# Kernel tuning notes

Measured on AMD Instinct MI355X. Metric: run time of the kernel, lower is better.

## Reference

```python
import jax, jax.numpy as jnp
import numpy as np

N_NODES = 100000
N_EDGES = 1600000
F_IN = 128
HIDDEN = 64
OUT = 1
NUM_GRAPHS = 128


def gcn_conv(x, src, dst, W, b, n_nodes):
    """PyG GCNConv: h = x @ W; add self-loops; symmetric deg normalization;
    scatter-add aggregation; + bias."""
    h = x @ W  # [N, H]
    ones = jnp.ones(src.shape[0], dtype=h.dtype)
    # degree on target nodes, +1 for the self-loop
    deg = jax.ops.segment_sum(ones, dst, num_segments=n_nodes) + 1.0  # [N]
    dinv = jax.lax.rsqrt(deg)  # deg^-0.5
    norm = dinv[src] * dinv[dst]  # [E]
    msg = h[src] * norm[:, None]  # gather + normalize, [E, H]
    agg = jax.ops.segment_sum(msg, dst, num_segments=n_nodes)  # scatter-add
    # self-loop contribution: norm_ii = deg_i^-1
    agg = agg + h * (1.0 / deg)[:, None]
    return agg + b


def setup_inputs() -> dict:
    key = jax.random.key(0)
    ks = jax.random.split(key, 8)
    x = jax.random.normal(ks[0], (N_NODES, F_IN), dtype=jnp.float32)
    edge_index = jax.random.randint(ks[1], (2, N_EDGES), 0, N_NODES, dtype=jnp.int64)
    batch = jnp.sort(jax.random.randint(ks[2], (N_NODES,), 0, NUM_GRAPHS, dtype=jnp.int64))
    s1 = 1.0 / np.sqrt(F_IN)
    s2 = 1.0 / np.sqrt(HIDDEN)
    W1 = jax.random.uniform(ks[3], (F_IN, HIDDEN), jnp.float32, -s1, s1)
    b1 = jnp.zeros((HIDDEN,), jnp.float32)
    W2 = jax.random.uniform(ks[4], (HIDDEN, HIDDEN), jnp.float32, -s2, s2)
    b2 = jnp.zeros((HIDDEN,), jnp.float32)
    W_out = jax.random.uniform(ks[5], (HIDDEN, OUT), jnp.float32, -s2, s2)
    b_out = jnp.zeros((OUT,), jnp.float32)
    return {"x": x, "edge_index": edge_index, "batch": batch,
            "W1": W1, "b1": b1, "W2": W2, "b2": b2,
            "W_out": W_out, "b_out": b_out}


def reference(x, edge_index, batch, W1, b1, W2, b2, W_out, b_out):
    n_nodes = x.shape[0]
    src, dst = edge_index[0], edge_index[1]
    h = jax.nn.relu(gcn_conv(x, src, dst, W1, b1, n_nodes))
    h = jax.nn.relu(gcn_conv(h, src, dst, W2, b2, n_nodes))
    # global mean pool over graphs
    sums = jax.ops.segment_sum(h, batch, num_segments=NUM_GRAPHS)  # [G, H]
    counts = jax.ops.segment_sum(jnp.ones(n_nodes, h.dtype), batch, num_segments=NUM_GRAPHS)
    pooled = sums / jnp.maximum(counts, 1.0)[:, None]
    return pooled @ W_out + b_out  # [G, 1]
```

## Files before the change

### kernel.cpp

```cpp
#include <hip/hip_runtime.h>
#include <hip/hip_fp16.h>

#define N_NODES 100000
#define N_EDGES 1600000
#define F_IN 128
#define HID 64
#define NG 128

#define GEMB 1563
#define DEGB 6250
#define CNTB 391
#define NB   391

#define FMA_ROW(acc, xv) \
    acc.x = fmaf(xv.x, w0.x, acc.x); acc.y = fmaf(xv.x, w0.y, acc.y); \
    acc.z = fmaf(xv.x, w0.z, acc.z); acc.w = fmaf(xv.x, w0.w, acc.w); \
    acc.x = fmaf(xv.y, w1.x, acc.x); acc.y = fmaf(xv.y, w1.y, acc.y); \
    acc.z = fmaf(xv.y, w1.z, acc.z); acc.w = fmaf(xv.y, w1.w, acc.w); \
    acc.x = fmaf(xv.z, w2.x, acc.x); acc.y = fmaf(xv.z, w2.y, acc.y); \
    acc.z = fmaf(xv.z, w2.z, acc.z); acc.w = fmaf(xv.z, w2.w, acc.w); \
    acc.x = fmaf(xv.w, w3.x, acc.x); acc.y = fmaf(xv.w, w3.y, acc.y); \
    acc.z = fmaf(xv.w, w3.z, acc.z); acc.w = fmaf(xv.w, w3.w, acc.w);

#define FMA_EDGE(hh, ww) \
    acc.x = fmaf(hh.x, ww, acc.x); acc.y = fmaf(hh.y, ww, acc.y); \
    acc.z = fmaf(hh.z, ww, acc.z); acc.w = fmaf(hh.w, ww, acc.w);

#define ADD_EDGE(hh) \
    acc.x += hh.x; acc.y += hh.y; acc.z += hh.z; acc.w += hh.w;

__device__ __forceinline__ float4 ldh4(const __half* p) {
    uint2 u = *(const uint2*)p;
    __half2 a = *(__half2*)&u.x, b = *(__half2*)&u.y;
    float2 fa = __half22float2(a), fb = __half22float2(b);
    return make_float4(fa.x, fa.y, fb.x, fb.y);
}
__device__ __forceinline__ void sth4(__half* p, float4 v) {
    __half2 a = __floats2half2_rn(v.x, v.y), b = __floats2half2_rn(v.z, v.w);
    uint2 u; u.x = *(unsigned int*)&a; u.y = *(unsigned int*)&b;
    *(uint2*)p = u;
}

__device__ __forceinline__ float4 gather_row_w(const __half* __restrict__ h16,
                                               const int* __restrict__ eidx,
                                               const float* __restrict__ dinv,
                                               int e0, int e1, int c4) {
    float4 acc = make_float4(0.f, 0.f, 0.f, 0.f);
    int e = e0;
    for (; e + 7 < e1; e += 8) {
        int s0 = eidx[e],     s1 = eidx[e + 1], s2 = eidx[e + 2], s3 = eidx[e + 3];
        int s4 = eidx[e + 4], s5 = eidx[e + 5], s6 = eidx[e + 6], s7 = eidx[e + 7];
        float w0 = dinv[s0], w1 = dinv[s1], w2 = dinv[s2], w3 = dinv[s3];
        float w4 = dinv[s4], w5 = dinv[s5], w6 = dinv[s6], w7 = dinv[s7];
        float4 h0 = ldh4(&h16[(size_t)s0 * HID + c4]);
        float4 h1 = ldh4(&h16[(size_t)s1 * HID + c4]);
        float4 h2 = ldh4(&h16[(size_t)s2 * HID + c4]);
        float4 h3 = ldh4(&h16[(size_t)s3 * HID + c4]);
        float4 h4 = ldh4(&h16[(size_t)s4 * HID + c4]);
        float4 h5 = ldh4(&h16[(size_t)s5 * HID + c4]);
        float4 h6 = ldh4(&h16[(size_t)s6 * HID + c4]);
        float4 h7 = ldh4(&h16[(size_t)s7 * HID + c4]);
        FMA_EDGE(h0, w0); FMA_EDGE(h1, w1); FMA_EDGE(h2, w2); FMA_EDGE(h3, w3);
        FMA_EDGE(h4, w4); FMA_EDGE(h5, w5); FMA_EDGE(h6, w6); FMA_EDGE(h7, w7);
    }
    if (e + 3 < e1) {
        int s0 = eidx[e], s1 = eidx[e + 1], s2 = eidx[e + 2], s3 = eidx[e + 3];
        float w0 = dinv[s0], w1 = dinv[s1], w2 = dinv[s2], w3 = dinv[s3];
        float4 h0 = ldh4(&h16[(size_t)s0 * HID + c4]);
        float4 h1 = ldh4(&h16[(size_t)s1 * HID + c4]);
        float4 h2 = ldh4(&h16[(size_t)s2 * HID + c4]);
        float4 h3 = ldh4(&h16[(size_t)s3 * HID + c4]);
        FMA_EDGE(h0, w0); FMA_EDGE(h1, w1); FMA_EDGE(h2, w2); FMA_EDGE(h3, w3);
        e += 4;
    }
    for (; e < e1; ++e) {
        int s0 = eidx[e];
        float w0 = dinv[s0];
        float4 h0 = ldh4(&h16[(size_t)s0 * HID + c4]);
        FMA_EDGE(h0, w0);
    }
    return acc;
}

__device__ __forceinline__ float4 gather_row_nw(const __half* __restrict__ h16,
                                                const int* __restrict__ eidx,
                                                int e0, int e1, int c4) {
    float4 acc = make_float4(0.f, 0.f, 0.f, 0.f);
    int e = e0;
    for (; e + 7 < e1; e += 8) {
        int s0 = eidx[e],     s1 = eidx[e + 1], s2 = eidx[e + 2], s3 = eidx[e + 3];
        int s4 = eidx[e + 4], s5 = eidx[e + 5], s6 = eidx[e + 6], s7 = eidx[e + 7];
        float4 h0 = ldh4(&h16[(size_t)s0 * HID + c4]);
        float4 h1 = ldh4(&h16[(size_t)s1 * HID + c4]);
        float4 h2 = ldh4(&h16[(size_t)s2 * HID + c4]);
        float4 h3 = ldh4(&h16[(size_t)s3 * HID + c4]);
        float4 h4 = ldh4(&h16[(size_t)s4 * HID + c4]);
        float4 h5 = ldh4(&h16[(size_t)s5 * HID + c4]);
        float4 h6 = ldh4(&h16[(size_t)s6 * HID + c4]);
        float4 h7 = ldh4(&h16[(size_t)s7 * HID + c4]);
        ADD_EDGE(h0); ADD_EDGE(h1); ADD_EDGE(h2); ADD_EDGE(h3);
        ADD_EDGE(h4); ADD_EDGE(h5); ADD_EDGE(h6); ADD_EDGE(h7);
    }
    if (e + 3 < e1) {
        int s0 = eidx[e], s1 = eidx[e + 1], s2 = eidx[e + 2], s3 = eidx[e + 3];
        float4 h0 = ldh4(&h16[(size_t)s0 * HID + c4]);
        float4 h1 = ldh4(&h16[(size_t)s1 * HID + c4]);
        float4 h2 = ldh4(&h16[(size_t)s2 * HID + c4]);
        float4 h3 = ldh4(&h16[(size_t)s3 * HID + c4]);
        ADD_EDGE(h0); ADD_EDGE(h1); ADD_EDGE(h2); ADD_EDGE(h3);
        e += 4;
    }
    for (; e < e1; ++e) {
        int s0 = eidx[e];
        float4 h0 = ldh4(&h16[(size_t)s0 * HID + c4]);
        ADD_EDGE(h0);
    }
    return acc;
}

template <int K>
__device__ __forceinline__ void gemm_tile(const float* __restrict__ X,
                                          const float* __restrict__ W,
                                          __half* __restrict__ H16,
                                          int tile, float* smem) {
    const int tid = threadIdx.x;
    const int rg  = tid >> 4;
    const int c4  = (tid & 15) * 4;
    const int r0  = tile * 64 + rg * 4;
    const bool full = (r0 + 3 < N_NODES);

    float4 a0 = {0,0,0,0}, a1 = {0,0,0,0}, a2 = {0,0,0,0}, a3 = {0,0,0,0};

    for (int kh = 0; kh < K; kh += 64) {
        __syncthreads();
        for (int i = tid; i < 1024; i += 256)
            ((float4*)smem)[i] = ((const float4*)(W + kh * 64))[i];
        __syncthreads();

        const float* Xb = X + (size_t)r0 * K + kh;
        #pragma unroll 4
        for (int k2 = 0; k2 < 64; k2 += 4) {
            float4 w0 = *(float4*)&smem[(k2 + 0) * 64 + c4];
            float4 w1 = *(float4*)&smem[(k2 + 1) * 64 + c4];
            float4 w2 = *(float4*)&smem[(k2 + 2) * 64 + c4];
            float4 w3 = *(float4*)&smem[(k2 + 3) * 64 + c4];
            float4 x0 = {0,0,0,0}, x1 = {0,0,0,0}, x2 = {0,0,0,0}, x3 = {0,0,0,0};
            if (full) {
                x0 = *(const float4*)&Xb[0 * (size_t)K + k2];
                x1 = *(const float4*)&Xb[1 * (size_t)K + k2];
                x2 = *(const float4*)&Xb[2 * (size_t)K + k2];
                x3 = *(const float4*)&Xb[3 * (size_t)K + k2];
            } else {
                if (r0 + 0 < N_NODES) x0 = *(const float4*)&Xb[0 * (size_t)K + k2];
                if (r0 + 1 < N_NODES) x1 = *(const float4*)&Xb[1 * (size_t)K + k2];
                if (r0 + 2 < N_NODES) x2 = *(const float4*)&Xb[2 * (size_t)K + k2];
                if (r0 + 3 < N_NODES) x3 = *(const float4*)&Xb[3 * (size_t)K + k2];
            }
            FMA_ROW(a0, x0);
            FMA_ROW(a1, x1);
            FMA_ROW(a2, x2);
            FMA_ROW(a3, x3);
        }
    }

    if (full) {
        sth4(&H16[(size_t)(r0 + 0) * HID + c4], a0);
        sth4(&H16[(size_t)(r0 + 1) * HID + c4], a1);
        sth4(&H16[(size_t)(r0 + 2) * HID + c4], a2);
        sth4(&H16[(size_t)(r0 + 3) * HID + c4], a3);
    } else {
        if (r0 + 0 < N_NODES) sth4(&H16[(size_t)(r0 + 0) * HID + c4], a0);
        if (r0 + 1 < N_NODES) sth4(&H16[(size_t)(r0 + 1) * HID + c4], a1);
        if (r0 + 2 < N_NODES) sth4(&H16[(size_t)(r0 + 2) * HID + c4], a2);
        if (r0 + 3 < N_NODES) sth4(&H16[(size_t)(r0 + 3) * HID + c4], a3);
    }
}

__global__ __launch_bounds__(256) void k_front(const int* __restrict__ dst,
                                               int* __restrict__ deg,
                                               int* __restrict__ rank,
                                               const int* __restrict__ batch,
                                               int* __restrict__ gcnt,
                                               const float* __restrict__ X,
                                               const float* __restrict__ W,
                                               __half* __restrict__ H16) {
    __shared__ float smem[4096];
    int bid = blockIdx.x;
    if (bid < GEMB) {
        gemm_tile<F_IN>(X, W, H16, bid, smem);
    } else if (bid < GEMB + DEGB) {
        int e = (bid - GEMB) * 256 + threadIdx.x;
        if (e < N_EDGES) rank[e] = atomicAdd(&deg[dst[e]], 1);
    } else {
        int* bins = (int*)smem;
        if (threadIdx.x < NG) bins[threadIdx.x] = 0;
        __syncthreads();
        int i = (bid - GEMB - DEGB) * 256 + threadIdx.x;
        if (i < N_NODES) atomicAdd(&bins[batch[i]], 1);
        __syncthreads();
        if (threadIdx.x < NG && bins[threadIdx.x] != 0)
            atomicAdd(&gcnt[threadIdx.x], bins[threadIdx.x]);
    }
}

__global__ __launch_bounds__(256) void k_blocksum(const int* __restrict__ deg,
                                                  int* __restrict__ bsum) {
    __shared__ int red[256];
    int i = blockIdx.x * 256 + threadIdx.x;
    red[threadIdx.x] = (i < N_NODES) ? deg[i] : 0;
    __syncthreads();
    for (int off = 128; off > 0; off >>= 1) {
        if (threadIdx.x < off) red[threadIdx.x] += red[threadIdx.x + off];
        __syncthreads();
    }
    if (threadIdx.x == 0) bsum[blockIdx.x] = red[0];
}

__global__ __launch_bounds__(512) void k_scanb(const int* __restrict__ bsum,
                                               int* __restrict__ boff, int nb) {
    __shared__ int tmp[512];
    int t = threadIdx.x;
    int v = (t < nb) ? bsum[t] : 0;
    tmp[t] = v;
    __syncthreads();
    for (int off = 1; off < 512; off <<= 1) {
        int u = (t >= off) ? tmp[t - off] : 0;
        __syncthreads();
        tmp[t] += u;
        __syncthreads();
    }
    if (t < nb) boff[t] = tmp[t] - v;
}

__global__ __launch_bounds__(256) void k_scanfinal(const int* __restrict__ deg,
                                                   const int* __restrict__ boff,
                                                   int* __restrict__ rowptr,
                                                   float* __restrict__ dinv) {
    __shared__ int tmp[256];
    int i = blockIdx.x * 256 + threadIdx.x;
    int t = threadIdx.x;
    int v = (i < N_NODES) ? deg[i] : 0;
    tmp[t] = v;
    __syncthreads();
    for (int off = 1; off < 256; off <<= 1) {
        int u = (t >= off) ? tmp[t - off] : 0;
        __syncthreads();
        tmp[t] += u;
        __syncthreads();
    }
    int excl = boff[blockIdx.x] + tmp[t] - v;
    if (i < N_NODES) {
        rowptr[i] = excl;
        dinv[i] = 1.0f / sqrtf((float)v + 1.0f);
    }
    if (blockIdx.x == 0 && t == 0) rowptr[N_NODES] = N_EDGES;
}

__global__ __launch_bounds__(256) void k_fill(const int* __restrict__ src,
                                              const int* __restrict__ dst,
                                              const int* __restrict__ rank,
                                              const int* __restrict__ rowptr,
                                              int* __restrict__ eidx) {
    int e = blockIdx.x * 256 + threadIdx.x;
    if (e < N_EDGES) {
        eidx[rowptr[dst[e]] + rank[e]] = src[e];
    }
}

__global__ __launch_bounds__(256) void k_gathergemm(const __half* __restrict__ h16,
                                                    const int* __restrict__ eidx,
                                                    const int* __restrict__ rowptr,
                                                    const float* __restrict__ dinv,
                                                    const float* __restrict__ bias,
                                                    const float* __restrict__ W2,
                                                    __half* __restrict__ Hout16) {
    __shared__ float Xl[64][66];
    __shared__ float Wl[64 * 64];
    const int tid  = threadIdx.x;
    const int ng4  = tid >> 4;
    const int tile = blockIdx.x;
    const int c4   = (tid & 15) * 4;

    for (int i = tid; i < 64 * 16; i += 256)
        ((float4*)Wl)[i] = ((const float4*)W2)[i];

    float4 b = *(const float4*)&bias[c4];
    #pragma unroll
    for (int j = 0; j < 4; ++j) {
        int node = tile * 64 + ng4 * 4 + j;
        float4 r = make_float4(0.f, 0.f, 0.f, 0.f);
        if (node < N_NODES) {
            int e0 = rowptr[node], e1 = rowptr[node + 1];
            float4 acc = gather_row_w(h16, eidx, dinv, e0, e1, c4);
            float di = dinv[node];
            float4 hd = ldh4(&h16[(size_t)node * HID + c4]);
            r.x = fmaxf(fmaf(di, fmaf(di, hd.x, acc.x), b.x), 0.f);
            r.y = fmaxf(fmaf(di, fmaf(di, hd.y, acc.y), b.y), 0.f);
            r.z = fmaxf(fmaf(di, fmaf(di, hd.z, acc.z), b.z), 0.f);
            r.w = fmaxf(fmaf(di, fmaf(di, hd.w, acc.w), b.w), 0.f);
        }
        *(float4*)&Xl[ng4 * 4 + j][c4] = r;
    }
    __syncthreads();

    float4 a0 = {0,0,0,0}, a1 = {0,0,0,0}, a2 = {0,0,0,0}, a3 = {0,0,0,0};
    #pragma unroll 4
    for (int k2 = 0; k2 < 64; k2 += 4) {
        float4 w0 = *(float4*)&Wl[(k2 + 0) * 64 + c4];
        float4 w1 = *(float4*)&Wl[(k2 + 1) * 64 + c4];
        float4 w2 = *(float4*)&Wl[(k2 + 2) * 64 + c4];
        float4 w3 = *(float4*)&Wl[(k2 + 3) * 64 + c4];
        float4 x0 = *(float4*)&Xl[ng4 * 4 + 0][k2];
        float4 x1 = *(float4*)&Xl[ng4 * 4 + 1][k2];
        float4 x2 = *(float4*)&Xl[ng4 * 4 + 2][k2];
        float4 x3 = *(float4*)&Xl[ng4 * 4 + 3][k2];
        FMA_ROW(a0, x0);
        FMA_ROW(a1, x1);
        FMA_ROW(a2, x2);
        FMA_ROW(a3, x3);
    }

    const int r0 = tile * 64 + ng4 * 4;
    if (r0 + 0 < N_NODES) { float d0 = dinv[r0 + 0];
        a0.x *= d0; a0.y *= d0; a0.z *= d0; a0.w *= d0;
        sth4(&Hout16[(size_t)(r0 + 0) * HID + c4], a0); }
    if (r0 + 1 < N_NODES) { float d1 = dinv[r0 + 1];
        a1.x *= d1; a1.y *= d1; a1.z *= d1; a1.w *= d1;
        sth4(&Hout16[(size_t)(r0 + 1) * HID + c4], a1); }
    if (r0 + 2 < N_NODES) { float d2 = dinv[r0 + 2];
        a2.x *= d2; a2.y *= d2; a2.z *= d2; a2.w *= d2;
        sth4(&Hout16[(size_t)(r0 + 2) * HID + c4], a2); }
    if (r0 + 3 < N_NODES) { float d3 = dinv[r0 + 3];
        a3.x *= d3; a3.y *= d3; a3.z *= d3; a3.w *= d3;
        sth4(&Hout16[(size_t)(r0 + 3) * HID + c4], a3); }
}

__global__ __launch_bounds__(256) void k_gatherpool(const __half* __restrict__ hw16,
                                                    const int* __restrict__ eidx,
                                                    const int* __restrict__ rowptr,
                                                    const float* __restrict__ dinv,
                                                    const float* __restrict__ bias,
                                                    const int* __restrict__ batch,
                                                    float* __restrict__ gsum) {
    __shared__ float Xl[64][66];
    __shared__ int bl[64];
    const int tid  = threadIdx.x;
    const int ng4  = tid >> 4;
    const int tile = blockIdx.x;
    const int c4   = (tid & 15) * 4;

    if (tid < 64) {
        int node = tile * 64 + tid;
        bl[tid] = (node < N_NODES) ? batch[node] : -1;
    }

    float4 b = *(const float4*)&bias[c4];
    #pragma unroll
    for (int j = 0; j < 4; ++j) {
        int node = tile * 64 + ng4 * 4 + j;
        float4 r = make_float4(0.f, 0.f, 0.f, 0.f);
        if (node < N_NODES) {
            int e0 = rowptr[node], e1 = rowptr[node + 1];
            float4 acc = gather_row_nw(hw16, eidx, e0, e1, c4);
            float di = dinv[node];
            float4 hw = ldh4(&hw16[(size_t)node * HID + c4]);
            r.x = fmaxf(fmaf(di, acc.x + hw.x, b.x), 0.f);
            r.y = fmaxf(fmaf(di, acc.y + hw.y, b.y), 0.f);
            r.z = fmaxf(fmaf(di, acc.z + hw.z, b.z), 0.f);
            r.w = fmaxf(fmaf(di, acc.w + hw.w, b.w), 0.f);
        }
        *(float4*)&Xl[ng4 * 4 + j][c4] = r;
    }
    __syncthreads();

    if (tid < 64) {
        int c = tid;
        float acc = 0.f;
        int gprev = bl[0];
        #pragma unroll 8
        for (int n = 0; n < 64; ++n) {
            int g = bl[n];
            if (g < 0) break;
            if (g != gprev) {
                unsafeAtomicAdd(&gsum[gprev * HID + c], acc);
                acc = 0.f;
                gprev = g;
            }
            acc += Xl[n][c];
        }
        if (gprev >= 0) unsafeAtomicAdd(&gsum[gprev * HID + c], acc);
    }
}

__global__ void k_out(const float* __restrict__ gsum, const int* __restrict__ gcnt,
                      const float* __restrict__ Wout, const float* __restrict__ bout,
                      float* __restrict__ out) {
    int g = threadIdx.x;
    if (g >= NG) return;
    float acc = 0.f;
    for (int c = 0; c < HID; ++c) acc += gsum[g * HID + c] * Wout[c];
    float cnt = fmaxf((float)gcnt[g], 1.0f);
    out[g] = acc / cnt + bout[0];
}

extern "C" void kernel_launch(void* const* d_in, const int* in_sizes, int n_in,
                              void* d_out, int out_size, void* d_ws, size_t ws_size,
                              hipStream_t stream) {
    const float* x    = (const float*)d_in[0];
    const int*   ei   = (const int*)d_in[1];
    const int*   batch= (const int*)d_in[2];
    const float* W1   = (const float*)d_in[3];
    const float* b1   = (const float*)d_in[4];
    const float* W2   = (const float*)d_in[5];
    const float* b2   = (const float*)d_in[6];
    const float* Wout = (const float*)d_in[7];
    const float* bout = (const float*)d_in[8];
    float* out = (float*)d_out;

    const int* src  = ei;
    const int* dstp = ei + N_EDGES;

    char* w = (char*)d_ws;
    int*    deg   = (int*)w;    w += (size_t)N_NODES * 4;
    int*    gcnt  = (int*)w;    w += (size_t)NG * 4;
    int*    bsum  = (int*)w;    w += (size_t)512 * 4;
    int*    boff  = (int*)w;    w += (size_t)512 * 4;
    int*    rowptr= (int*)w;    w += (size_t)(N_NODES + 4) * 4;
    float*  dinv  = (float*)w;  w += (size_t)N_NODES * 4;
    float*  gsum  = (float*)w;  w += (size_t)NG * HID * 4;
    int*    rank  = (int*)w;    w += (size_t)N_EDGES * 4;
    int*    eidx  = (int*)w;    w += (size_t)N_EDGES * 4;
    __half* bufA16= (__half*)w; w += (size_t)N_NODES * HID * 2;
    __half* bufB16= (__half*)w; w += (size_t)N_NODES * HID * 2;

    hipMemsetAsync(deg,  0, (size_t)N_NODES * 4, stream);
    hipMemsetAsync(gcnt, 0, (size_t)NG * 4, stream);
    hipMemsetAsync(gsum, 0, (size_t)NG * HID * 4, stream);

    k_front<<<GEMB + DEGB + CNTB, 256, 0, stream>>>(dstp, deg, rank, batch, gcnt,
                                                    x, W1, bufA16);
    k_blocksum <<<NB, 256, 0, stream>>>(deg, bsum);
    k_scanb    <<<1, 512, 0, stream>>>(bsum, boff, NB);
    k_scanfinal<<<NB, 256, 0, stream>>>(deg, boff, rowptr, dinv);
    k_fill     <<<(N_EDGES + 255) / 256, 256, 0, stream>>>(src, dstp, rank, rowptr, eidx);

    k_gathergemm<<<GEMB, 256, 0, stream>>>(bufA16, eidx, rowptr, dinv, b1, W2, bufB16);

    k_gatherpool<<<GEMB, 256, 0, stream>>>(bufB16, eidx, rowptr, dinv, b2, batch, gsum);

    k_out<<<1, 128, 0, stream>>>(gsum, gcnt, Wout, bout, out);
}
```

Before: 273.7 us.

## Build CSR via two-level bucket sort instead of global atomic degree counting

Replaces per-edge global atomicAdd degree counting and the rank-based random scatter with a two-pass bucket sort. Edges are first binned by dst>>7 using per-block shared-memory histograms. After a scan they are scattered into buckets as packed (src<<7 | dst&127) records. Each bucket is then sorted locally in shared memory to produce rowptr, dinv and eidx. This removes contended global atomics and the rank array, at the cost of extra kernels and a local-capacity assumption of 4096 edges per bucket.

```diff
diff --git a/kernel.cpp b/kernel.cpp
--- a/kernel.cpp
+++ b/kernel.cpp
@@ -8,9 +8,10 @@
 #define NG 128
 
 #define GEMB 1563
-#define DEGB 6250
+#define NBINS 1024
+#define NBLK  391
+#define BUCKETS 782
 #define CNTB 391
-#define NB   391
 
 #define FMA_ROW(acc, xv) \
     acc.x = fmaf(xv.x, w0.x, acc.x); acc.y = fmaf(xv.x, w0.y, acc.y); \
@@ -177,8 +178,7 @@
 }
 
 __global__ __launch_bounds__(256) void k_front(const int* __restrict__ dst,
-                                               int* __restrict__ deg,
-                                               int* __restrict__ rank,
+                                               int* __restrict__ hist,
                                                const int* __restrict__ batch,
                                                int* __restrict__ gcnt,
                                                const float* __restrict__ X,
@@ -186,30 +186,45 @@
                                                __half* __restrict__ H16) {
     __shared__ float smem[4096];
     int bid = blockIdx.x;
+    int tid = threadIdx.x;
     if (bid < GEMB) {
         gemm_tile<F_IN>(X, W, H16, bid, smem);
-    } else if (bid < GEMB + DEGB) {
-        int e = (bid - GEMB) * 256 + threadIdx.x;
-        if (e < N_EDGES) rank[e] = atomicAdd(&deg[dst[e]], 1);
+    } else if (bid < GEMB + NBLK) {
+        int cb = bid - GEMB;
+        int* bins = (int*)smem;
+        for (int i = tid; i < NBINS; i += 256) bins[i] = 0;
+        __syncthreads();
+        #pragma unroll
+        for (int it = 0; it < 4; ++it) {
+            int base = cb * 4096 + it * 1024 + tid * 4;
+            if (base < N_EDGES) {
+                int4 d4 = *(const int4*)&dst[base];
+                atomicAdd(&bins[d4.x >> 7], 1);
+                atomicAdd(&bins[d4.y >> 7], 1);
+                atomicAdd(&bins[d4.z >> 7], 1);
+                atomicAdd(&bins[d4.w >> 7], 1);
+            }
+        }
+        __syncthreads();
+        for (int i = tid; i < NBINS; i += 256) hist[(size_t)i * NBLK + cb] = bins[i];
     } else {
         int* bins = (int*)smem;
-        if (threadIdx.x < NG) bins[threadIdx.x] = 0;
-        __syncthreads();
-        int i = (bid - GEMB - DEGB) * 256 + threadIdx.x;
+        if (tid < NG) bins[tid] = 0;
+        __syncthreads();
+        int i = (bid - GEMB - NBLK) * 256 + tid;
         if (i < N_NODES) atomicAdd(&bins[batch[i]], 1);
         __syncthreads();
-        if (threadIdx.x < NG && bins[threadIdx.x] != 0)
-            atomicAdd(&gcnt[threadIdx.x], bins[threadIdx.x]);
-    }
-}
-
-__global__ __launch_bounds__(256) void k_blocksum(const int* __restrict__ deg,
-                                                  int* __restrict__ bsum) {
-    __shared__ int red[256];
-    int i = blockIdx.x * 256 + threadIdx.x;
-    red[threadIdx.x] = (i < N_NODES) ? deg[i] : 0;
-    __syncthreads();
-    for (int off = 128; off > 0; off >>= 1) {
+        if (tid < NG && bins[tid] != 0) atomicAdd(&gcnt[tid], bins[tid]);
+    }
+}
+
+__global__ __launch_bounds__(1024) void k_bsum(const int* __restrict__ hist,
+                                               int* __restrict__ bsum) {
+    __shared__ int red[1024];
+    int i = blockIdx.x * 1024 + threadIdx.x;
+    red[threadIdx.x] = hist[i];
+    __syncthreads();
+    for (int off = 512; off > 0; off >>= 1) {
         if (threadIdx.x < off) red[threadIdx.x] += red[threadIdx.x + off];
         __syncthreads();
     }
@@ -232,39 +247,99 @@
     if (t < nb) boff[t] = tmp[t] - v;
 }
 
-__global__ __launch_bounds__(256) void k_scanfinal(const int* __restrict__ deg,
-                                                   const int* __restrict__ boff,
+__global__ __launch_bounds__(1024) void k_scanfin(int* __restrict__ hist,
+                                                  const int* __restrict__ boff,
+                                                  int* __restrict__ bucketstart) {
+    __shared__ int tmp[1024];
+    int i = blockIdx.x * 1024 + threadIdx.x;
+    int t = threadIdx.x;
+    int v = hist[i];
+    tmp[t] = v;
+    __syncthreads();
+    for (int off = 1; off < 1024; off <<= 1) {
+        int u = (t >= off) ? tmp[t - off] : 0;
+        __syncthreads();
+        tmp[t] += u;
+        __syncthreads();
+    }
+    int excl = boff[blockIdx.x] + tmp[t] - v;
+    hist[i] = excl;
+    if (i % NBLK == 0) bucketstart[i / NBLK] = excl;
+}
+
+__global__ __launch_bounds__(256) void k_scatter(const int* __restrict__ src,
+                                                 const int* __restrict__ dst,
+                                                 const int* __restrict__ hist,
+                                                 int* __restrict__ ebuf) {
+    __shared__ int cur[NBINS];
+    int cb = blockIdx.x;
+    int tid = threadIdx.x;
+    for (int i = tid; i < NBINS; i += 256) cur[i] = hist[(size_t)i * NBLK + cb];
+    __syncthreads();
+    #pragma unroll
+    for (int it = 0; it < 4; ++it) {
+        int base = cb * 4096 + it * 1024 + tid * 4;
+        if (base < N_EDGES) {
+            int4 s4 = *(const int4*)&src[base];
+            int4 d4 = *(const int4*)&dst[base];
+            int p0 = atomicAdd(&cur[d4.x >> 7], 1);
+            int p1 = atomicAdd(&cur[d4.y >> 7], 1);
+            int p2 = atomicAdd(&cur[d4.z >> 7], 1);
+            int p3 = atomicAdd(&cur[d4.w >> 7], 1);
+            ebuf[p0] = (s4.x << 7) | (d4.x & 127);
+            ebuf[p1] = (s4.y << 7) | (d4.y & 127);
+            ebuf[p2] = (s4.z << 7) | (d4.z & 127);
+            ebuf[p3] = (s4.w << 7) | (d4.w & 127);
+        }
+    }
+}
+
+__global__ __launch_bounds__(256) void k_bucketcsr(int* __restrict__ eidx,
+                                                   const int* __restrict__ bucketstart,
                                                    int* __restrict__ rowptr,
                                                    float* __restrict__ dinv) {
-    __shared__ int tmp[256];
-    int i = blockIdx.x * 256 + threadIdx.x;
-    int t = threadIdx.x;
-    int v = (i < N_NODES) ? deg[i] : 0;
-    tmp[t] = v;
-    __syncthreads();
-    for (int off = 1; off < 256; off <<= 1) {
-        int u = (t >= off) ? tmp[t - off] : 0;
-        __syncthreads();
-        tmp[t] += u;
-        __syncthreads();
-    }
-    int excl = boff[blockIdx.x] + tmp[t] - v;
-    if (i < N_NODES) {
-        rowptr[i] = excl;
-        dinv[i] = 1.0f / sqrtf((float)v + 1.0f);
-    }
-    if (blockIdx.x == 0 && t == 0) rowptr[N_NODES] = N_EDGES;
-}
-
-__global__ __launch_bounds__(256) void k_fill(const int* __restrict__ src,
-                                              const int* __restrict__ dst,
-                                              const int* __restrict__ rank,
-                                              const int* __restrict__ rowptr,
-                                              int* __restrict__ eidx) {
-    int e = blockIdx.x * 256 + threadIdx.x;
-    if (e < N_EDGES) {
-        eidx[rowptr[dst[e]] + rank[e]] = src[e];
-    }
+    __shared__ int lrec[4096];
+    __shared__ int lcnt[128];
+    __shared__ int lsum[128];
+    __shared__ int lcur[128];
+    int b = blockIdx.x;
+    int tid = threadIdx.x;
+    int s0 = bucketstart[b], s1 = bucketstart[b + 1];
+    int cnt = s1 - s0;
+
+    if (tid < 128) lcnt[tid] = 0;
+    __syncthreads();
+    for (int i = tid; i < cnt; i += 256) {
+        int r = eidx[s0 + i];
+        lrec[i] = r;
+        atomicAdd(&lcnt[r & 127], 1);
+    }
+    __syncthreads();
+    if (tid < 128) lsum[tid] = lcnt[tid];
+    __syncthreads();
+    for (int off = 1; off < 128; off <<= 1) {
+        int u = 0;
+        if (tid < 128 && tid >= off) u = lsum[tid - off];
+        __syncthreads();
+        if (tid < 128) lsum[tid] += u;
+        __syncthreads();
+    }
+    if (tid < 128) {
+        int excl = lsum[tid] - lcnt[tid];
+        lcur[tid] = s0 + excl;
+        int node = b * 128 + tid;
+        if (node < N_NODES) {
+            rowptr[node] = s0 + excl;
+            dinv[node] = 1.0f / sqrtf((float)lcnt[tid] + 1.0f);
+        }
+    }
+    __syncthreads();
+    for (int i = tid; i < cnt; i += 256) {
+        int r = lrec[i];
+        int p = atomicAdd(&lcur[r & 127], 1);
+        eidx[p] = r >> 7;
+    }
+    if (b == 0 && tid == 0) rowptr[N_NODES] = N_EDGES;
 }
 
 __global__ __launch_bounds__(256) void k_gathergemm(const __half* __restrict__ h16,
@@ -421,31 +496,30 @@
     const int* dstp = ei + N_EDGES;
 
     char* w = (char*)d_ws;
-    int*    deg   = (int*)w;    w += (size_t)N_NODES * 4;
+    int*    hist  = (int*)w;    w += (size_t)NBINS * NBLK * 4;
+    int*    bstrt = (int*)w;    w += (size_t)(NBINS + 8) * 4;
     int*    gcnt  = (int*)w;    w += (size_t)NG * 4;
     int*    bsum  = (int*)w;    w += (size_t)512 * 4;
     int*    boff  = (int*)w;    w += (size_t)512 * 4;
     int*    rowptr= (int*)w;    w += (size_t)(N_NODES + 4) * 4;
     float*  dinv  = (float*)w;  w += (size_t)N_NODES * 4;
     float*  gsum  = (float*)w;  w += (size_t)NG * HID * 4;
-    int*    rank  = (int*)w;    w += (size_t)N_EDGES * 4;
     int*    eidx  = (int*)w;    w += (size_t)N_EDGES * 4;
     __half* bufA16= (__half*)w; w += (size_t)N_NODES * HID * 2;
     __half* bufB16= (__half*)w; w += (size_t)N_NODES * HID * 2;
 
-    hipMemsetAsync(deg,  0, (size_t)N_NODES * 4, stream);
     hipMemsetAsync(gcnt, 0, (size_t)NG * 4, stream);
     hipMemsetAsync(gsum, 0, (size_t)NG * HID * 4, stream);
 
-    k_front<<<GEMB + DEGB + CNTB, 256, 0, stream>>>(dstp, deg, rank, batch, gcnt,
+    k_front<<<GEMB + NBLK + CNTB, 256, 0, stream>>>(dstp, hist, batch, gcnt,
                                                     x, W1, bufA16);
-    k_blocksum <<<NB, 256, 0, stream>>>(deg, bsum);
-    k_scanb    <<<1, 512, 0, stream>>>(bsum, boff, NB);
-    k_scanfinal<<<NB, 256, 0, stream>>>(deg, boff, rowptr, dinv);
-    k_fill     <<<(N_EDGES + 255) / 256, 256, 0, stream>>>(src, dstp, rank, rowptr, eidx);
+    k_bsum   <<<NBLK, 1024, 0, stream>>>(hist, bsum);
+    k_scanb  <<<1, 512, 0, stream>>>(bsum, boff, NBLK);
+    k_scanfin<<<NBLK, 1024, 0, stream>>>(hist, boff, bstrt);
+    k_scatter<<<NBLK, 256, 0, stream>>>(src, dstp, hist, eidx);
+    k_bucketcsr<<<BUCKETS, 256, 0, stream>>>(eidx, bstrt, rowptr, dinv);
 
     k_gathergemm<<<GEMB, 256, 0, stream>>>(bufA16, eidx, rowptr, dinv, b1, W2, bufB16);
-
     k_gatherpool<<<GEMB, 256, 0, stream>>>(bufB16, eidx, rowptr, dinv, b2, batch, gsum);
 
     k_out<<<1, 128, 0, stream>>>(gsum, gcnt, Wout, bout, out);
```

After: 226.7 us. -17.2%, faster.
